# Kernel tuning notes

Hardware: AMD Instinct MI355X
Metric: run time of the kernel (lower is better)

The kernel has to match this reference:

```python
import jax, jax.numpy as jnp
import numpy as np

N = 50000
E = 800000
IN = 256
HID = 64
HEADS = 4
EPS = 1e-5


def batchnorm(x, g, b):
    # training-mode BatchNorm1d over node dim, biased variance (torch semantics)
    mu = jnp.mean(x, axis=0)
    var = jnp.mean((x - mu) ** 2, axis=0)
    return (x - mu) * jax.lax.rsqrt(var + EPS) * g + b


def gat(x, edge_index, W, a_src, a_dst, bias, heads, out_ch, num_nodes):
    src, dst = edge_index[0], edge_index[1]
    h = (x @ W).reshape(num_nodes, heads, out_ch)          # [N,H,C]
    al_s = jnp.einsum('nhc,hc->nh', h, a_src)              # [N,H]
    al_d = jnp.einsum('nhc,hc->nh', h, a_dst)
    e = jax.nn.leaky_relu(al_s[src] + al_d[dst], 0.2)      # [E,H]
    # segment softmax over destination neighborhoods
    m = jax.ops.segment_max(e, dst, num_segments=num_nodes)
    m = jnp.where(jnp.isfinite(m), m, 0.0)
    ex = jnp.exp(e - m[dst])                               # [E,H]
    denom = jax.ops.segment_sum(ex, dst, num_segments=num_nodes)
    alpha = ex / (denom[dst] + 1e-16)                      # [E,H]
    msg = alpha[:, :, None] * h[src]                       # [E,H,C]
    out = jax.ops.segment_sum(msg, dst, num_segments=num_nodes)
    return out.reshape(num_nodes, heads * out_ch) + bias


def setup_inputs() -> dict:
    key = jax.random.key(0)
    ks = jax.random.split(key, 12)
    d = {}
    d['x'] = jax.random.normal(ks[0], (N, IN), jnp.float32)
    d['edge_index'] = jax.random.randint(ks[1], (2, E), 0, N, jnp.int32)
    d['bn1_g'] = jnp.ones((IN,), jnp.float32)
    d['bn1_b'] = jnp.zeros((IN,), jnp.float32)
    d['lin1_W'] = jax.random.normal(ks[2], (IN, HID * HEADS), jnp.float32) * (1.0 / np.sqrt(IN))
    d['lin1_b'] = jnp.zeros((HID * HEADS,), jnp.float32)
    d['con1_W'] = jax.random.normal(ks[3], (IN, HID * HEADS), jnp.float32) * (1.0 / np.sqrt(IN))
    d['con1_asrc'] = jax.random.normal(ks[4], (HEADS, HID), jnp.float32) * 0.1
    d['con1_adst'] = jax.random.normal(ks[5], (HEADS, HID), jnp.float32) * 0.1
    d['con1_b'] = jnp.zeros((HID * HEADS,), jnp.float32)
    d['bn3_g'] = jnp.ones((HID * HEADS,), jnp.float32)
    d['bn3_b'] = jnp.zeros((HID * HEADS,), jnp.float32)
    d['lin3_W'] = jax.random.normal(ks[6], (HID * HEADS, 2), jnp.float32) * (1.0 / np.sqrt(HID * HEADS))
    d['lin3_b'] = jnp.zeros((2,), jnp.float32)
    d['con3_W'] = jax.random.normal(ks[7], (HID * HEADS, 2), jnp.float32) * (1.0 / np.sqrt(HID * HEADS))
    d['con3_asrc'] = jax.random.normal(ks[8], (1, 2), jnp.float32) * 0.1
    d['con3_adst'] = jax.random.normal(ks[9], (1, 2), jnp.float32) * 0.1
    d['con3_b'] = jnp.zeros((2,), jnp.float32)
    return d


def reference(x, edge_index, bn1_g, bn1_b, lin1_W, lin1_b, con1_W, con1_asrc, con1_adst, con1_b,
              bn3_g, bn3_b, lin3_W, lin3_b, con3_W, con3_asrc, con3_adst, con3_b):
    x = batchnorm(x, bn1_g, bn1_b)
    x = jax.nn.relu(x @ lin1_W + lin1_b
                    + gat(x, edge_index, con1_W, con1_asrc, con1_adst, con1_b, HEADS, HID, N))
    x = batchnorm(x, bn3_g, bn3_b)
    x = jax.nn.relu(x @ lin3_W + lin3_b
                    + gat(x, edge_index, con3_W, con3_asrc, con3_adst, con3_b, 1, 2, N))
    return x
```

## Files before the change

kernel.cpp:

```cpp
#include <hip/hip_runtime.h>
#include <math.h>

#define NN 50000
#define NE 800000
#define IC 256
#define EPS 1e-5f

typedef __attribute__((ext_vector_type(8))) short short8;
typedef __attribute__((ext_vector_type(4))) float f32x4;

enum : int {
  OFF_S1     = 0,
  OFF_S2     = 256,
  OFF_COUNTS = 512,
  ZERO_END   = OFF_COUNTS + 50000,
  OFF_CURSOR = ZERO_END,
  OFF_START  = OFF_CURSOR + 50000,
  OFF_BSUM   = OFF_START + 50004,
  OFF_BOFF   = OFF_BSUM + 64,
  OFF_ALS    = OFF_BOFF + 64,
  OFF_ALD    = OFF_ALS + 200000,
  OFF_SRCS   = OFF_ALD + 200000,
  OFF_Y32    = OFF_SRCS + 800000,
  OFF_ND4    = OFF_Y32 + 100000,
  OFF_BFH    = OFF_ND4 + 200000,
  OFF_HBF    = OFF_BFH + 65536,
  OFF_YLBF   = OFF_HBF + 6400000,
  WS_FLOATS  = OFF_YLBF + 6400000
};

__device__ __forceinline__ float lrelu(float s) { return s > 0.f ? s : 0.2f * s; }
__device__ __forceinline__ float b2f(unsigned short u) {
  return __uint_as_float(((unsigned)u) << 16);
}
__device__ __forceinline__ unsigned short f2bf(float f) {
  unsigned u = __float_as_uint(f);
  return (unsigned short)((u + 0x7fffu + ((u >> 16) & 1u)) >> 16);
}

__global__ __launch_bounds__(256) void k_prep(const float* __restrict__ x,
                                              float* __restrict__ S1,
                                              float* __restrict__ S2,
                                              const int* __restrict__ dst,
                                              int* __restrict__ counts,
                                              const float* __restrict__ Wlin,
                                              const float* __restrict__ Wcon,
                                              unsigned short* __restrict__ Bfh) {
  int b = blockIdx.x;
  if (b < 1024) {
    int c = threadIdx.x;
    float s1 = 0.f, s2 = 0.f;
    for (int r = b; r < NN; r += 1024) {
      float v = x[r * IC + c];
      s1 += v;
      s2 = fmaf(v, v, s2);
    }
    atomicAdd(&S1[c], s1);
    atomicAdd(&S2[c], s2);
  } else if (b < 4149) {
    int e = (b - 1024) * 256 + threadIdx.x;
    atomicAdd(&counts[dst[e]], 1);
  } else {
    int id = (b - 4149) * 256 + threadIdx.x;
    int j = id & 7, lane = (id >> 3) & 63, nt = (id >> 9) & 31, ks = id >> 14;
    int k = ks * 32 + ((lane >> 4) << 3) + j;
    int n = nt * 16 + (lane & 15);
    float v = (n < 256) ? Wlin[k * 256 + n] : Wcon[k * 256 + (n - 256)];
    Bfh[id] = f2bf(v);
  }
}

__global__ __launch_bounds__(256) void k_bnstats2(const unsigned short* __restrict__ x1,
                                                  float* __restrict__ S1,
                                                  float* __restrict__ S2) {
  int c = threadIdx.x;
  float s1 = 0.f, s2 = 0.f;
  for (int r = blockIdx.x; r < NN; r += gridDim.x) {
    float v = b2f(x1[r * IC + c]);
    s1 += v;
    s2 = fmaf(v, v, s2);
  }
  atomicAdd(&S1[c], s1);
  atomicAdd(&S2[c], s2);
}

__global__ __launch_bounds__(256, 4) void k_gemm(const float* __restrict__ x,
                                                 const float* __restrict__ S1,
                                                 const float* __restrict__ S2,
                                                 const float* __restrict__ bng,
                                                 const float* __restrict__ bnb,
                                                 const unsigned short* __restrict__ Bfh,
                                                 unsigned short* __restrict__ ylbf,
                                                 unsigned short* __restrict__ hbf,
                                                 const float* __restrict__ asrc,
                                                 const float* __restrict__ adst,
                                                 float* __restrict__ als,
                                                 float* __restrict__ ald) {
  __shared__ unsigned short Ah[2048];
  __shared__ float sc[256], sh[256];
  const int tid = threadIdx.x;
  const int bn = blockIdx.x;
  const int row0 = blockIdx.y * 64;
  const int wave = tid >> 6, lane = tid & 63;
  {
    float mu = S1[tid] * (1.f / NN);
    float var = S2[tid] * (1.f / NN) - mu * mu;
    float ss = bng[tid] / sqrtf(var + EPS);
    sc[tid] = ss;
    sh[tid] = bnb[tid] - mu * ss;
  }
  const float4* x4 = (const float4*)x;
  const short8* Bh8 = (const short8*)Bfh;
  f32x4 acc[4][4];
#pragma unroll
  for (int i = 0; i < 4; ++i)
#pragma unroll
    for (int j = 0; j < 4; ++j) acc[i][j] = (f32x4){0.f, 0.f, 0.f, 0.f};

  const int m = tid >> 2, kg = tid & 3;
  const int r = row0 + m;
  const int aaddr = (((m >> 4) * 64) + ((m & 15) | (kg << 4))) * 8;
  __syncthreads();

  for (int ks = 0; ks < 8; ++ks) {
    const int c0 = ks * 32 + kg * 8;
    float v[8];
    if (r < NN) {
      int base = (r * IC + c0) >> 2;
      float4 fa = x4[base], fb = x4[base + 1];
      v[0] = fa.x; v[1] = fa.y; v[2] = fa.z; v[3] = fa.w;
      v[4] = fb.x; v[5] = fb.y; v[6] = fb.z; v[7] = fb.w;
#pragma unroll
      for (int j = 0; j < 8; ++j) v[j] = fmaf(v[j], sc[c0 + j], sh[c0 + j]);
    } else {
#pragma unroll
      for (int j = 0; j < 8; ++j) v[j] = 0.f;
    }
    unsigned ph[4];
#pragma unroll
    for (int j = 0; j < 4; ++j) {
      ph[j] = (unsigned)f2bf(v[2 * j]) | ((unsigned)f2bf(v[2 * j + 1]) << 16);
    }
    *(uint4*)&Ah[aaddr] = make_uint4(ph[0], ph[1], ph[2], ph[3]);
    __syncthreads();

    short8 ah[4];
#pragma unroll
    for (int mt = 0; mt < 4; ++mt)
      ah[mt] = *(const short8*)&Ah[(mt * 64 + lane) * 8];
#pragma unroll
    for (int nt = 0; nt < 4; ++nt) {
      short8 bh = Bh8[(ks * 32 + bn * 16 + wave * 4 + nt) * 64 + lane];
#pragma unroll
      for (int mt = 0; mt < 4; ++mt)
        acc[mt][nt] = __builtin_amdgcn_mfma_f32_16x16x32_bf16(ah[mt], bh, acc[mt][nt], 0, 0, 0);
    }
    __syncthreads();
  }
  const int colq = lane & 15, quad = lane >> 4;
  if (bn == 0) {
#pragma unroll
    for (int mt = 0; mt < 4; ++mt)
#pragma unroll
      for (int reg = 0; reg < 4; ++reg) {
        int rr = row0 + mt * 16 + quad * 4 + reg;
        if (rr < NN) {
#pragma unroll
          for (int nt = 0; nt < 4; ++nt)
            ylbf[rr * IC + wave * 64 + nt * 16 + colq] = f2bf(acc[mt][nt][reg]);
        }
      }
  } else {
    const int head = wave;
    float asv[4], adv[4];
#pragma unroll
    for (int j = 0; j < 4; ++j) {
      asv[j] = asrc[head * 64 + j * 16 + colq];
      adv[j] = adst[head * 64 + j * 16 + colq];
    }
#pragma unroll
    for (int mt = 0; mt < 4; ++mt)
#pragma unroll
      for (int reg = 0; reg < 4; ++reg) {
        int rr = row0 + mt * 16 + quad * 4 + reg;
        float sA = 0.f, dA = 0.f;
#pragma unroll
        for (int j = 0; j < 4; ++j) {
          float hA = acc[mt][j][reg];
          sA = fmaf(hA, asv[j], sA);
          dA = fmaf(hA, adv[j], dA);
          if (rr < NN) hbf[rr * IC + head * 64 + j * 16 + colq] = f2bf(hA);
        }
#pragma unroll
        for (int off = 1; off < 16; off <<= 1) {
          sA += __shfl_xor(sA, off, 64);
          dA += __shfl_xor(dA, off, 64);
        }
        if (rr < NN) {
          if (colq == 0) als[rr * 4 + head] = sA;
          else if (colq == 1) ald[rr * 4 + head] = dA;
        }
      }
  }
}

__global__ __launch_bounds__(1024) void k_scan(const int* __restrict__ counts,
                                               int* __restrict__ start,
                                               int* __restrict__ cursor,
                                               float* __restrict__ S1,
                                               float* __restrict__ S2) {
  __shared__ int red[16];
  __shared__ int buf[1024];
  const int tid = threadIdx.x, b = blockIdx.x;
  const int base = b * 1024;
  int pre = 0;
  for (int i = tid; i < base; i += 1024) pre += counts[i];
#pragma unroll
  for (int off = 1; off < 64; off <<= 1) pre += __shfl_xor(pre, off, 64);
  if ((tid & 63) == 0) red[tid >> 6] = pre;
  if (b == 0 && tid < 256) {
    S1[tid] = 0.f;
    S2[tid] = 0.f;
  }
  __syncthreads();
  int bpre = 0;
#pragma unroll
  for (int w = 0; w < 16; ++w) bpre += red[w];
  int i = base + tid;
  int v = (i < NN) ? counts[i] : 0;
  buf[tid] = v;
  __syncthreads();
  for (int off = 1; off < 1024; off <<= 1) {
    int t = (tid >= off) ? buf[tid - off] : 0;
    __syncthreads();
    buf[tid] += t;
    __syncthreads();
  }
  if (i < NN) {
    int s = bpre + buf[tid] - v;
    start[i] = s;
    cursor[i] = s;
  }
  if (b == 48 && tid == 1023) start[NN] = bpre + buf[1023];
}

__global__ __launch_bounds__(256) void k_scatter(const int* __restrict__ src,
                                                 const int* __restrict__ dst,
                                                 int* __restrict__ cursor,
                                                 int* __restrict__ srcs) {
  int e = blockIdx.x * 256 + threadIdx.x;
  int pos = atomicAdd(&cursor[dst[e]], 1);
  srcs[pos] = src[e];
}

__global__ __launch_bounds__(256) void k_agg(const ushort4* __restrict__ hq,
                                             ushort4* __restrict__ x1,
                                             const float4* __restrict__ als4,
                                             const float4* __restrict__ ald4,
                                             const int* __restrict__ start,
                                             const int* __restrict__ srcs,
                                             const float4* __restrict__ lb4,
                                             const float4* __restrict__ cb4) {
  __shared__ float lsp[1024];
  const int tid = threadIdx.x;
  const int wave = tid >> 6, lane = tid & 63, head = lane >> 4;
  const int n = blockIdx.x * 4 + wave;
  const float* als = (const float*)als4;
  const int s = start[n], t = start[n + 1];
  const int deg = t - s;
  const float4 aldv = ald4[n];
  int svk = -1;
  float p0 = 0.f, p1 = 0.f, p2 = 0.f, p3 = 0.f;
  if (lane < deg) {
    svk = srcs[s + lane];
    float4 a = als4[svk];
    p0 = __expf(lrelu(a.x + aldv.x));
    p1 = __expf(lrelu(a.y + aldv.y));
    p2 = __expf(lrelu(a.z + aldv.z));
    p3 = __expf(lrelu(a.w + aldv.w));
  }
  *(float4*)&lsp[wave * 256 + lane * 4] = make_float4(p0, p1, p2, p3);
  float d0 = p0, d1 = p1, d2 = p2, d3 = p3;
  const float aldh = head == 0 ? aldv.x : head == 1 ? aldv.y : head == 2 ? aldv.z : aldv.w;
  if (deg > 64) {
    for (int i = s + 64 + lane; i < t; i += 64) {
      float4 a = als4[srcs[i]];
      d0 += __expf(lrelu(a.x + aldv.x));
      d1 += __expf(lrelu(a.y + aldv.y));
      d2 += __expf(lrelu(a.z + aldv.z));
      d3 += __expf(lrelu(a.w + aldv.w));
    }
  }
#pragma unroll
  for (int off = 1; off < 64; off <<= 1) {
    d0 += __shfl_xor(d0, off, 64);
    d1 += __shfl_xor(d1, off, 64);
    d2 += __shfl_xor(d2, off, 64);
    d3 += __shfl_xor(d3, off, 64);
  }
  const float inv =
      1.f / ((head == 0 ? d0 : head == 1 ? d1 : head == 2 ? d2 : d3) + 1e-16f);
  float a0 = 0.f, a1 = 0.f, a2 = 0.f, a3 = 0.f;
  const int cnt = min(deg, 64);
  const int wbase = wave * 256 + head;
  int j = 0;
  for (; j + 4 <= cnt; j += 4) {
    int sv0 = __shfl(svk, j, 64), sv1 = __shfl(svk, j + 1, 64);
    int sv2 = __shfl(svk, j + 2, 64), sv3 = __shfl(svk, j + 3, 64);
    ushort4 hv0 = hq[sv0 * 64 + lane];
    ushort4 hv1 = hq[sv1 * 64 + lane];
    ushort4 hv2 = hq[sv2 * 64 + lane];
    ushort4 hv3 = hq[sv3 * 64 + lane];
    float w0 = lsp[wbase + j * 4], w1 = lsp[wbase + j * 4 + 4];
    float w2 = lsp[wbase + j * 4 + 8], w3 = lsp[wbase + j * 4 + 12];
    a0 = fmaf(w0, b2f(hv0.x), a0); a1 = fmaf(w0, b2f(hv0.y), a1);
    a2 = fmaf(w0, b2f(hv0.z), a2); a3 = fmaf(w0, b2f(hv0.w), a3);
    a0 = fmaf(w1, b2f(hv1.x), a0); a1 = fmaf(w1, b2f(hv1.y), a1);
    a2 = fmaf(w1, b2f(hv1.z), a2); a3 = fmaf(w1, b2f(hv1.w), a3);
    a0 = fmaf(w2, b2f(hv2.x), a0); a1 = fmaf(w2, b2f(hv2.y), a1);
    a2 = fmaf(w2, b2f(hv2.z), a2); a3 = fmaf(w2, b2f(hv2.w), a3);
    a0 = fmaf(w3, b2f(hv3.x), a0); a1 = fmaf(w3, b2f(hv3.y), a1);
    a2 = fmaf(w3, b2f(hv3.z), a2); a3 = fmaf(w3, b2f(hv3.w), a3);
  }
  for (; j < cnt; ++j) {
    int sv = __shfl(svk, j, 64);
    float w = lsp[wbase + j * 4];
    ushort4 hv = hq[sv * 64 + lane];
    a0 = fmaf(w, b2f(hv.x), a0);
    a1 = fmaf(w, b2f(hv.y), a1);
    a2 = fmaf(w, b2f(hv.z), a2);
    a3 = fmaf(w, b2f(hv.w), a3);
  }
  if (deg > 64) {
    for (int i = s + 64; i < t; ++i) {
      int sv = srcs[i];
      float av = als[sv * 4 + head];
      float p = __expf(lrelu(av + aldh));
      ushort4 hv = hq[sv * 64 + lane];
      a0 = fmaf(p, b2f(hv.x), a0);
      a1 = fmaf(p, b2f(hv.y), a1);
      a2 = fmaf(p, b2f(hv.z), a2);
      a3 = fmaf(p, b2f(hv.w), a3);
    }
  }
  ushort4 yb = x1[n * 64 + lane];
  float4 bb1 = lb4[lane], bb2 = cb4[lane];
  ushort4 rb;
  rb.x = f2bf(fmaxf(fmaf(a0, inv, b2f(yb.x) + bb1.x + bb2.x), 0.f));
  rb.y = f2bf(fmaxf(fmaf(a1, inv, b2f(yb.y) + bb1.y + bb2.y), 0.f));
  rb.z = f2bf(fmaxf(fmaf(a2, inv, b2f(yb.z) + bb1.z + bb2.z), 0.f));
  rb.w = f2bf(fmaxf(fmaf(a3, inv, b2f(yb.w) + bb1.w + bb2.w), 0.f));
  x1[n * 64 + lane] = rb;
}

__global__ __launch_bounds__(256) void k_node2(const ushort4* __restrict__ x1,
                                               const float* __restrict__ S1,
                                               const float* __restrict__ S2,
                                               const float* __restrict__ g3,
                                               const float* __restrict__ b3,
                                               const float4* __restrict__ Wl4,
                                               const float4* __restrict__ Wc4,
                                               const float* __restrict__ a3s,
                                               const float* __restrict__ a3d,
                                               const float* __restrict__ l3b,
                                               const float* __restrict__ c3b,
                                               float2* __restrict__ y32,
                                               float4* __restrict__ nd4) {
  __shared__ float sc[256], sh[256];
  const int tid = threadIdx.x;
  {
    float mu = S1[tid] * (1.f / NN);
    float var = S2[tid] * (1.f / NN) - mu * mu;
    float ss = g3[tid] / sqrtf(var + EPS);
    sc[tid] = ss;
    sh[tid] = b3[tid] - mu * ss;
  }
  __syncthreads();
  const int n = blockIdx.x * 4 + (tid >> 6);
  const int lane = tid & 63;
  ushort4 xb = x1[n * 64 + lane];
  float x0 = fmaf(b2f(xb.x), sc[lane * 4 + 0], sh[lane * 4 + 0]);
  float x1v = fmaf(b2f(xb.y), sc[lane * 4 + 1], sh[lane * 4 + 1]);
  float x2 = fmaf(b2f(xb.z), sc[lane * 4 + 2], sh[lane * 4 + 2]);
  float x3 = fmaf(b2f(xb.w), sc[lane * 4 + 3], sh[lane * 4 + 3]);
  float4 wa = Wl4[lane * 2], wb = Wl4[lane * 2 + 1];
  float y0 = x0 * wa.x + x1v * wa.z + x2 * wb.x + x3 * wb.z;
  float y1 = x0 * wa.y + x1v * wa.w + x2 * wb.y + x3 * wb.w;
  float4 ca = Wc4[lane * 2], cb = Wc4[lane * 2 + 1];
  float g0 = x0 * ca.x + x1v * ca.z + x2 * cb.x + x3 * cb.z;
  float g1 = x0 * ca.y + x1v * ca.w + x2 * cb.y + x3 * cb.w;
#pragma unroll
  for (int off = 1; off < 64; off <<= 1) {
    y0 += __shfl_xor(y0, off, 64);
    y1 += __shfl_xor(y1, off, 64);
    g0 += __shfl_xor(g0, off, 64);
    g1 += __shfl_xor(g1, off, 64);
  }
  if (lane == 0) {
    y32[n] = make_float2(y0 + l3b[0] + c3b[0], y1 + l3b[1] + c3b[1]);
    nd4[n] = make_float4(g0 * a3s[0] + g1 * a3s[1], g0, g1,
                         g0 * a3d[0] + g1 * a3d[1]);
  }
}

__global__ __launch_bounds__(256) void k_final(const int* __restrict__ start,
                                               const int* __restrict__ srcs,
                                               const float4* __restrict__ nd4,
                                               const float2* __restrict__ y32,
                                               float* __restrict__ out) {
  const int tid = threadIdx.x;
  const int n = blockIdx.x * 16 + (tid >> 4);
  const int li = tid & 15;
  const int s = start[n], t = start[n + 1];
  const float ad = nd4[n].w;
  float den = 0.f, a0 = 0.f, a1 = 0.f;
  for (int ii = s + li; ii < t; ii += 16) {
    float4 vv = nd4[srcs[ii]];
    float p = __expf(lrelu(vv.x + ad));
    den += p;
    a0 = fmaf(p, vv.y, a0);
    a1 = fmaf(p, vv.z, a1);
  }
#pragma unroll
  for (int off = 1; off < 16; off <<= 1) {
    den += __shfl_xor(den, off, 64);
    a0 += __shfl_xor(a0, off, 64);
    a1 += __shfl_xor(a1, off, 64);
  }
  if (li == 0) {
    float2 y = y32[n];
    float inv = 1.f / (den + 1e-16f);
    out[2 * n] = fmaxf(fmaf(a0, inv, y.x), 0.f);
    out[2 * n + 1] = fmaxf(fmaf(a1, inv, y.y), 0.f);
  }
}

extern "C" void kernel_launch(void* const* d_in, const int* in_sizes, int n_in,
                              void* d_out, int out_size, void* d_ws, size_t ws_size,
                              hipStream_t stream) {
  const float* x = (const float*)d_in[0];
  const int* ei = (const int*)d_in[1];
  const float* bn1_g = (const float*)d_in[2];
  const float* bn1_b = (const float*)d_in[3];
  const float* lin1_W = (const float*)d_in[4];
  const float* lin1_b = (const float*)d_in[5];
  const float* con1_W = (const float*)d_in[6];
  const float* con1_as = (const float*)d_in[7];
  const float* con1_ad = (const float*)d_in[8];
  const float* con1_b = (const float*)d_in[9];
  const float* bn3_g = (const float*)d_in[10];
  const float* bn3_b = (const float*)d_in[11];
  const float* lin3_W = (const float*)d_in[12];
  const float* lin3_b = (const float*)d_in[13];
  const float* con3_W = (const float*)d_in[14];
  const float* con3_as = (const float*)d_in[15];
  const float* con3_ad = (const float*)d_in[16];
  const float* con3_b = (const float*)d_in[17];
  float* ws = (float*)d_ws;
  const int* srcA = ei;
  const int* dstA = ei + NE;

  float* S1 = ws + OFF_S1;
  float* S2 = ws + OFF_S2;
  int* counts = (int*)(ws + OFF_COUNTS);
  int* cursor = (int*)(ws + OFF_CURSOR);
  int* start = (int*)(ws + OFF_START);
  float* als = ws + OFF_ALS;
  float* ald = ws + OFF_ALD;
  int* srcs = (int*)(ws + OFF_SRCS);
  float2* y32 = (float2*)(ws + OFF_Y32);
  float4* nd4 = (float4*)(ws + OFF_ND4);
  unsigned short* Bfh = (unsigned short*)(ws + OFF_BFH);
  unsigned short* hbf = (unsigned short*)(ws + OFF_HBF);
  unsigned short* ylbf = (unsigned short*)(ws + OFF_YLBF);

  hipMemsetAsync(ws, 0, (size_t)ZERO_END * sizeof(float), stream);

  k_prep<<<4661, 256, 0, stream>>>(x, S1, S2, dstA, counts, lin1_W, con1_W, Bfh);
  k_gemm<<<dim3(2, 782), 256, 0, stream>>>(x, S1, S2, bn1_g, bn1_b, Bfh, ylbf, hbf,
                                           con1_as, con1_ad, als, ald);
  k_scan<<<49, 1024, 0, stream>>>(counts, start, cursor, S1, S2);
  k_scatter<<<3125, 256, 0, stream>>>(srcA, dstA, cursor, srcs);
  k_agg<<<12500, 256, 0, stream>>>((const ushort4*)hbf, (ushort4*)ylbf,
                                   (const float4*)als, (const float4*)ald, start,
                                   srcs, (const float4*)lin1_b,
                                   (const float4*)con1_b);
  k_bnstats2<<<1024, 256, 0, stream>>>(ylbf, S1, S2);
  k_node2<<<12500, 256, 0, stream>>>((const ushort4*)ylbf, S1, S2, bn3_g, bn3_b,
                                     (const float4*)lin3_W, (const float4*)con3_W,
                                     con3_as, con3_ad, lin3_b, con3_b, y32, nd4);
  k_final<<<3125, 256, 0, stream>>>(start, srcs, nd4, y32, (float*)d_out);
}
```

Before: 413.0 us.

## Fuse CSR prefix scan into GEMM launch and use packed bf16 conversion

The separate k_scan kernel is folded into k_gemm as 49 extra leading blocks. Each of these runs a 256-thread scan using wave shuffles over four counts per thread, in place of the 1024-thread shared-memory Hillis-Steele loop. The GEMM blocks are remapped from a 2D grid to a 1D grid with an 8-row swizzle so both column halves of a row tile run close together and share cached x rows. The bf16 packing uses the v_cvt_pk_bf16_f32 instruction, and S1/S2 zeroing moves into k_scatter. k_agg is split into two half-size launches, which adds one launch and does not obviously help.

```diff
diff --git a/kernel.cpp b/kernel.cpp
--- a/kernel.cpp
+++ b/kernel.cpp
@@ -37,6 +37,11 @@
   unsigned u = __float_as_uint(f);
   return (unsigned short)((u + 0x7fffu + ((u >> 16) & 1u)) >> 16);
 }
+__device__ __forceinline__ unsigned cvtpk(float lo, float hi) {
+  unsigned r;
+  asm("v_cvt_pk_bf16_f32 %0, %1, %2" : "=v"(r) : "v"(lo), "v"(hi));
+  return r;
+}
 
 __global__ __launch_bounds__(256) void k_prep(const float* __restrict__ x,
                                               float* __restrict__ S1,
@@ -95,12 +100,56 @@
                                                  const float* __restrict__ asrc,
                                                  const float* __restrict__ adst,
                                                  float* __restrict__ als,
-                                                 float* __restrict__ ald) {
+                                                 float* __restrict__ ald,
+                                                 const int* __restrict__ counts,
+                                                 int* __restrict__ start,
+                                                 int* __restrict__ cursor) {
+  const int tid = threadIdx.x;
+  const int b = blockIdx.x;
+  if (b < 56) {
+    if (b >= 49) return;
+    __shared__ int red[4], wsum[4];
+    const int lane = tid & 63, wv = tid >> 6;
+    const int base = b << 10;
+    int pre = 0;
+    for (int i = tid; i < base; i += 256) pre += counts[i];
+#pragma unroll
+    for (int off = 1; off < 64; off <<= 1) pre += __shfl_xor(pre, off, 64);
+    if (lane == 0) red[wv] = pre;
+    const int i0 = base + tid * 4;
+    int c0 = (i0 < NN) ? counts[i0] : 0;
+    int c1 = (i0 + 1 < NN) ? counts[i0 + 1] : 0;
+    int c2 = (i0 + 2 < NN) ? counts[i0 + 2] : 0;
+    int c3 = (i0 + 3 < NN) ? counts[i0 + 3] : 0;
+    const int tsum = c0 + c1 + c2 + c3;
+    int isc = tsum;
+#pragma unroll
+    for (int off = 1; off < 64; off <<= 1) {
+      int t = __shfl_up(isc, off, 64);
+      if (lane >= off) isc += t;
+    }
+    if (lane == 63) wsum[wv] = isc;
+    __syncthreads();
+    int ex = red[0] + red[1] + red[2] + red[3] + (isc - tsum);
+    for (int w = 0; w < wv; ++w) ex += wsum[w];
+    if (i0 < NN) { start[i0] = ex; cursor[i0] = ex; }
+    ex += c0;
+    if (i0 + 1 < NN) { start[i0 + 1] = ex; cursor[i0 + 1] = ex; }
+    ex += c1;
+    if (i0 + 2 < NN) { start[i0 + 2] = ex; cursor[i0 + 2] = ex; }
+    ex += c2;
+    if (i0 + 3 < NN) { start[i0 + 3] = ex; cursor[i0 + 3] = ex; }
+    ex += c3;
+    if (b == 48 && tid == 255) start[NN] = ex;
+    return;
+  }
+  const int g = b - 56;
+  const int row_blk = (g >> 4) * 8 + (g & 7);
+  const int bn = (g >> 3) & 1;
+  if (row_blk >= 782) return;
+  const int row0 = row_blk * 64;
   __shared__ unsigned short Ah[2048];
   __shared__ float sc[256], sh[256];
-  const int tid = threadIdx.x;
-  const int bn = blockIdx.x;
-  const int row0 = blockIdx.y * 64;
   const int wave = tid >> 6, lane = tid & 63;
   {
     float mu = S1[tid] * (1.f / NN);
@@ -138,9 +187,7 @@
     }
     unsigned ph[4];
 #pragma unroll
-    for (int j = 0; j < 4; ++j) {
-      ph[j] = (unsigned)f2bf(v[2 * j]) | ((unsigned)f2bf(v[2 * j + 1]) << 16);
-    }
+    for (int j = 0; j < 4; ++j) ph[j] = cvtpk(v[2 * j], v[2 * j + 1]);
     *(uint4*)&Ah[aaddr] = make_uint4(ph[0], ph[1], ph[2], ph[3]);
     __syncthreads();
 
@@ -204,50 +251,16 @@
   }
 }
 
-__global__ __launch_bounds__(1024) void k_scan(const int* __restrict__ counts,
-                                               int* __restrict__ start,
-                                               int* __restrict__ cursor,
-                                               float* __restrict__ S1,
-                                               float* __restrict__ S2) {
-  __shared__ int red[16];
-  __shared__ int buf[1024];
-  const int tid = threadIdx.x, b = blockIdx.x;
-  const int base = b * 1024;
-  int pre = 0;
-  for (int i = tid; i < base; i += 1024) pre += counts[i];
-#pragma unroll
-  for (int off = 1; off < 64; off <<= 1) pre += __shfl_xor(pre, off, 64);
-  if ((tid & 63) == 0) red[tid >> 6] = pre;
-  if (b == 0 && tid < 256) {
-    S1[tid] = 0.f;
-    S2[tid] = 0.f;
-  }
-  __syncthreads();
-  int bpre = 0;
-#pragma unroll
-  for (int w = 0; w < 16; ++w) bpre += red[w];
-  int i = base + tid;
-  int v = (i < NN) ? counts[i] : 0;
-  buf[tid] = v;
-  __syncthreads();
-  for (int off = 1; off < 1024; off <<= 1) {
-    int t = (tid >= off) ? buf[tid - off] : 0;
-    __syncthreads();
-    buf[tid] += t;
-    __syncthreads();
-  }
-  if (i < NN) {
-    int s = bpre + buf[tid] - v;
-    start[i] = s;
-    cursor[i] = s;
-  }
-  if (b == 48 && tid == 1023) start[NN] = bpre + buf[1023];
-}
-
 __global__ __launch_bounds__(256) void k_scatter(const int* __restrict__ src,
                                                  const int* __restrict__ dst,
                                                  int* __restrict__ cursor,
-                                                 int* __restrict__ srcs) {
+                                                 int* __restrict__ srcs,
+                                                 float* __restrict__ S1,
+                                                 float* __restrict__ S2) {
+  if (blockIdx.x == 0) {
+    S1[threadIdx.x] = 0.f;
+    S2[threadIdx.x] = 0.f;
+  }
   int e = blockIdx.x * 256 + threadIdx.x;
   int pos = atomicAdd(&cursor[dst[e]], 1);
   srcs[pos] = src[e];
@@ -260,11 +273,12 @@
                                              const int* __restrict__ start,
                                              const int* __restrict__ srcs,
                                              const float4* __restrict__ lb4,
-                                             const float4* __restrict__ cb4) {
+                                             const float4* __restrict__ cb4,
+                                             const int nb0) {
   __shared__ float lsp[1024];
   const int tid = threadIdx.x;
   const int wave = tid >> 6, lane = tid & 63, head = lane >> 4;
-  const int n = blockIdx.x * 4 + wave;
+  const int n = nb0 + blockIdx.x * 4 + wave;
   const float* als = (const float*)als4;
   const int s = start[n], t = start[n + 1];
   const int deg = t - s;
@@ -477,14 +491,18 @@
   hipMemsetAsync(ws, 0, (size_t)ZERO_END * sizeof(float), stream);
 
   k_prep<<<4661, 256, 0, stream>>>(x, S1, S2, dstA, counts, lin1_W, con1_W, Bfh);
-  k_gemm<<<dim3(2, 782), 256, 0, stream>>>(x, S1, S2, bn1_g, bn1_b, Bfh, ylbf, hbf,
-                                           con1_as, con1_ad, als, ald);
-  k_scan<<<49, 1024, 0, stream>>>(counts, start, cursor, S1, S2);
-  k_scatter<<<3125, 256, 0, stream>>>(srcA, dstA, cursor, srcs);
-  k_agg<<<12500, 256, 0, stream>>>((const ushort4*)hbf, (ushort4*)ylbf,
-                                   (const float4*)als, (const float4*)ald, start,
-                                   srcs, (const float4*)lin1_b,
-                                   (const float4*)con1_b);
+  k_gemm<<<56 + 1568, 256, 0, stream>>>(x, S1, S2, bn1_g, bn1_b, Bfh, ylbf, hbf,
+                                        con1_as, con1_ad, als, ald, counts, start,
+                                        cursor);
+  k_scatter<<<3125, 256, 0, stream>>>(srcA, dstA, cursor, srcs, S1, S2);
+  k_agg<<<6250, 256, 0, stream>>>((const ushort4*)hbf, (ushort4*)ylbf,
+                                  (const float4*)als, (const float4*)ald, start,
+                                  srcs, (const float4*)lin1_b,
+                                  (const float4*)con1_b, 0);
+  k_agg<<<6250, 256, 0, stream>>>((const ushort4*)hbf, (ushort4*)ylbf,
+                                  (const float4*)als, (const float4*)ald, start,
+                                  srcs, (const float4*)lin1_b,
+                                  (const float4*)con1_b, 25000);
   k_bnstats2<<<1024, 256, 0, stream>>>(ylbf, S1, S2);
   k_node2<<<12500, 256, 0, stream>>>((const ushort4*)ylbf, S1, S2, bn3_g, bn3_b,
                                      (const float4*)lin3_W, (const float4*)con3_W,
```

New measurement: 407.7 us. No clear change (-1.3%).
